# Kernel tuning notes

Measured on AMD Instinct MI355X. Metric: run time of the kernel, lower is better.

The kernel has to match this reference:

```python
import jax, jax.numpy as jnp
import numpy as np

B, S, H, D = 4, 2048, 12, 64
WINDOW = 128          # local_attention window => (w//2, w//2) sliding window
BASE = 16000.0        # rope theta (ProkBert default)
NEG = -1e9


def rotate_half(x):
    x1, x2 = jnp.split(x, 2, axis=-1)
    return jnp.concatenate([-x2, x1], axis=-1)


def setup_inputs() -> dict:
    key = jax.random.key(0)
    k1, = jax.random.split(key, 1)
    qkv = jax.random.normal(k1, (B, S, 3, H, D), dtype=jnp.float32)
    pos = jnp.arange(S)
    inv_freq = 1.0 / (BASE ** (jnp.arange(0, D, 2).astype(jnp.float32) / D))
    freqs = pos[:, None].astype(jnp.float32) * inv_freq[None, :]   # (S, D/2)
    emb = jnp.concatenate([freqs, freqs], axis=-1)                  # (S, D)
    cos = jnp.cos(emb)
    sin = jnp.sin(emb)
    dist = jnp.abs(pos[:, None] - pos[None, :])
    mask = jnp.where(dist <= WINDOW // 2, 0.0, NEG).astype(jnp.float32)[None, None]  # (1,1,S,S)
    return {"qkv": qkv, "cos": cos, "sin": sin, "mask": mask}


def reference(qkv, cos, sin, mask):
    # qkv: (B, S, 3, H, D) -> q/k/v: (B, H, S, D)
    q = jnp.swapaxes(qkv[:, :, 0], 1, 2)
    k = jnp.swapaxes(qkv[:, :, 1], 1, 2)
    v = jnp.swapaxes(qkv[:, :, 2], 1, 2)
    cos_b = cos[None, None]   # (1,1,S,D)
    sin_b = sin[None, None]
    q = q * cos_b + rotate_half(q) * sin_b
    k = k * cos_b + rotate_half(k) * sin_b
    scale = D ** -0.5
    scores = jnp.einsum('bhqd,bhkd->bhqk', q, k) * scale + mask
    w = jax.nn.softmax(scores.astype(jnp.float32), axis=-1).astype(q.dtype)
    out = jnp.einsum('bhqk,bhkd->bhqd', w, v)
    out = jnp.swapaxes(out, 1, 2).reshape(B, S, H * D)  # (B, S, dim)
    return out
```

## Files before the change

kernel.cpp:

```cpp
#include <hip/hip_runtime.h>
#include <hip/hip_bf16.h>
#include <cstdint>


typedef short bf16x8 __attribute__((ext_vector_type(8)));
typedef float f32x4  __attribute__((ext_vector_type(4)));
typedef uint32_t u32x4 __attribute__((ext_vector_type(4)));

#define SLEN   2048
#define NHEAD  12
#define NBATCH 4
#define HD     64
#define WHALF  64
#define QT     64
#define KROWS  192
#define NKC    9
#define VST    68
#define VROWS  96
#define QSCALE 0.18033688011112042f


__device__ __forceinline__ uint32_t cvt_pk(float lo, float hi) {
    uint32_t r;
    asm("v_cvt_pk_bf16_f32 %0, %1, %2" : "=v"(r) : "v"(lo), "v"(hi));
    return r;
}

__global__ __launch_bounds__(256, 3) void prokbert_attn(
        const float* __restrict__ qkv, const float* __restrict__ cosT,
        const float* __restrict__ sinT, float* __restrict__ out)
{
    __shared__ __align__(16) short    sK[KROWS * 64];
    __shared__ __align__(16) uint32_t sV[VROWS * VST];

    const int tid = threadIdx.x;

    const int bid = blockIdx.x;
    const int gid = (bid & 7) * 192 + (bid >> 3);
    const int qt = gid & 31;
    const int hh = gid >> 5;
    const int h = hh % NHEAD, b = hh / NHEAD;

    const int q0 = qt * QT;
    const int kstart = q0 - WHALF;

    const int wv = tid >> 6;
    const int lane = tid & 63;
    const int r = lane & 15, g = lane >> 4;
    const int rx = r & 7;
    const int qrow = q0 + wv * 16 + r;

    f32x4 va[3][2], vb[3][2];
    #pragma unroll
    for (int it = 0; it < 3; ++it) {
        const int j = tid + it * 256;
        const int kp = j >> 3, dd = (j & 7) * 8;
        const int s0 = kstart + 2 * kp, s1 = s0 + 1;
        const f32x4 z = {0.f, 0.f, 0.f, 0.f};
        if ((unsigned)s0 < SLEN) {
            const f32x4* g0 = (const f32x4*)(qkv +
                (((size_t)(b * SLEN + s0) * 3 + 2) * NHEAD + h) * HD + dd);
            va[it][0] = g0[0]; va[it][1] = g0[1];
        } else { va[it][0] = z; va[it][1] = z; }
        if ((unsigned)s1 < SLEN) {
            const f32x4* g1 = (const f32x4*)(qkv +
                (((size_t)(b * SLEN + s1) * 3 + 2) * NHEAD + h) * HD + dd);
            vb[it][0] = g1[0]; vb[it][1] = g1[1];
        } else { vb[it][0] = z; vb[it][1] = z; }
    }

    const int rrb = tid >> 2, c4 = tid & 3, d0 = c4 * 8;

#define LOADK(IT, S) \
    f32x4 xl0##S, xl1##S, xh0##S, xh1##S, cc0##S, cc1##S, ss0##S, ss1##S; \
    { \
        const int s = kstart + rrb + (IT) * 64; \
        if ((unsigned)s < SLEN) { \
            const size_t kbase = (((size_t)(b * SLEN + s) * 3 + 1) * NHEAD + h) * HD; \
            const f32x4* gxl = (const f32x4*)(qkv + kbase + d0); \
            const f32x4* gxh = (const f32x4*)(qkv + kbase + d0 + 32); \
            const f32x4* gc  = (const f32x4*)(cosT + s * HD + d0); \
            const f32x4* gs  = (const f32x4*)(sinT + s * HD + d0); \
            xl0##S = gxl[0]; xl1##S = gxl[1]; \
            xh0##S = gxh[0]; xh1##S = gxh[1]; \
            cc0##S = gc[0];  cc1##S = gc[1]; \
            ss0##S = gs[0];  ss1##S = gs[1]; \
        } else { \
            const f32x4 z = {0.f, 0.f, 0.f, 0.f}; \
            xl0##S = z; xl1##S = z; xh0##S = z; xh1##S = z; \
            cc0##S = z; cc1##S = z; ss0##S = z; ss1##S = z; \
        } \
    }

#define CONVSTOREK(IT, S) \
    { \
        const int rr = rrb + (IT) * 64; \
        u32x4 klo, khi; \
         \
        klo[0] = cvt_pk(xl0##S[0] * cc0##S[0] - xh0##S[0] * ss0##S[0], \
                        xl0##S[1] * cc0##S[1] - xh0##S[1] * ss0##S[1]); \
        klo[1] = cvt_pk(xl0##S[2] * cc0##S[2] - xh0##S[2] * ss0##S[2], \
                        xl0##S[3] * cc0##S[3] - xh0##S[3] * ss0##S[3]); \
        klo[2] = cvt_pk(xl1##S[0] * cc1##S[0] - xh1##S[0] * ss1##S[0], \
                        xl1##S[1] * cc1##S[1] - xh1##S[1] * ss1##S[1]); \
        klo[3] = cvt_pk(xl1##S[2] * cc1##S[2] - xh1##S[2] * ss1##S[2], \
                        xl1##S[3] * cc1##S[3] - xh1##S[3] * ss1##S[3]); \
        khi[0] = cvt_pk(xh0##S[0] * cc0##S[0] + xl0##S[0] * ss0##S[0], \
                        xh0##S[1] * cc0##S[1] + xl0##S[1] * ss0##S[1]); \
        khi[1] = cvt_pk(xh0##S[2] * cc0##S[2] + xl0##S[2] * ss0##S[2], \
                        xh0##S[3] * cc0##S[3] + xl0##S[3] * ss0##S[3]); \
        khi[2] = cvt_pk(xh1##S[0] * cc1##S[0] + xl1##S[0] * ss1##S[0], \
                        xh1##S[1] * cc1##S[1] + xl1##S[1] * ss1##S[1]); \
        khi[3] = cvt_pk(xh1##S[2] * cc1##S[2] + xl1##S[2] * ss1##S[2], \
                        xh1##S[3] * cc1##S[3] + xl1##S[3] * ss1##S[3]); \
        const int sw = rr & 7; \
        *(u32x4*)&sK[rr * 64 + ((c4 ^ sw) << 3)]       = klo; \
        *(u32x4*)&sK[rr * 64 + (((c4 + 4) ^ sw) << 3)] = khi; \
    }

    {
        LOADK(0, a)
        LOADK(1, bb)
        CONVSTOREK(0, a)
        LOADK(2, cc)
        CONVSTOREK(1, bb)
        CONVSTOREK(2, cc)
    }
#undef LOADK
#undef CONVSTOREK

    bf16x8 qf0, qf1;
    {
        const size_t qb = (((size_t)(b * SLEN + qrow) * 3 + 0) * NHEAD + h) * HD;
        const f32x4* ga  = (const f32x4*)(qkv + qb + g * 8);
        const f32x4* gb  = (const f32x4*)(qkv + qb + 32 + g * 8);
        const f32x4* gc0 = (const f32x4*)(cosT + (size_t)qrow * HD + g * 8);
        const f32x4* gs0 = (const f32x4*)(sinT + (size_t)qrow * HD + g * 8);
        f32x4 qa0 = ga[0], qa1 = ga[1], qb0 = gb[0], qb1 = gb[1];
        f32x4 qc0 = gc0[0], qc1 = gc0[1], qs0 = gs0[0], qs1 = gs0[1];
        u32x4 w0, w1;
        w0[0] = cvt_pk((qa0[0] * qc0[0] - qb0[0] * qs0[0]) * QSCALE,
                       (qa0[1] * qc0[1] - qb0[1] * qs0[1]) * QSCALE);
        w0[1] = cvt_pk((qa0[2] * qc0[2] - qb0[2] * qs0[2]) * QSCALE,
                       (qa0[3] * qc0[3] - qb0[3] * qs0[3]) * QSCALE);
        w0[2] = cvt_pk((qa1[0] * qc1[0] - qb1[0] * qs1[0]) * QSCALE,
                       (qa1[1] * qc1[1] - qb1[1] * qs1[1]) * QSCALE);
        w0[3] = cvt_pk((qa1[2] * qc1[2] - qb1[2] * qs1[2]) * QSCALE,
                       (qa1[3] * qc1[3] - qb1[3] * qs1[3]) * QSCALE);
        w1[0] = cvt_pk((qb0[0] * qc0[0] + qa0[0] * qs0[0]) * QSCALE,
                       (qb0[1] * qc0[1] + qa0[1] * qs0[1]) * QSCALE);
        w1[1] = cvt_pk((qb0[2] * qc0[2] + qa0[2] * qs0[2]) * QSCALE,
                       (qb0[3] * qc0[3] + qa0[3] * qs0[3]) * QSCALE);
        w1[2] = cvt_pk((qb1[0] * qc1[0] + qa1[0] * qs1[0]) * QSCALE,
                       (qb1[1] * qc1[1] + qa1[1] * qs1[1]) * QSCALE);
        w1[3] = cvt_pk((qb1[2] * qc1[2] + qa1[2] * qs1[2]) * QSCALE,
                       (qb1[3] * qc1[3] + qa1[3] * qs1[3]) * QSCALE);
        qf0 = __builtin_bit_cast(bf16x8, w0);
        qf1 = __builtin_bit_cast(bf16x8, w1);
    }

    #pragma unroll
    for (int it = 0; it < 3; ++it) {
        const int j = tid + it * 256;
        const int kp = j >> 3, dd = (j & 7) * 8;
        u32x4 w0, w1;
        w0[0] = cvt_pk(va[it][0][0], vb[it][0][0]);
        w0[1] = cvt_pk(va[it][0][1], vb[it][0][1]);
        w0[2] = cvt_pk(va[it][0][2], vb[it][0][2]);
        w0[3] = cvt_pk(va[it][0][3], vb[it][0][3]);
        w1[0] = cvt_pk(va[it][1][0], vb[it][1][0]);
        w1[1] = cvt_pk(va[it][1][1], vb[it][1][1]);
        w1[2] = cvt_pk(va[it][1][2], vb[it][1][2]);
        w1[3] = cvt_pk(va[it][1][3], vb[it][1][3]);
        *(u32x4*)&sV[kp * VST + dd]     = w0;
        *(u32x4*)&sV[kp * VST + dd + 4] = w1;
    }

    __syncthreads();

    u32x4 paw[5];
    float sum = 0.f;
    const int tg = 4 * g;
    #pragma unroll
    for (int kc = 0; kc < NKC; ++kc) {
        const int row = wv * 16 + kc * 16 + r;
        const bf16x8 ka0 = *(const bf16x8*)&sK[row * 64 + ((g ^ rx) << 3)];
        const bf16x8 ka1 = *(const bf16x8*)&sK[row * 64 + (((g + 4) ^ rx) << 3)];
        f32x4 c = {0.f, 0.f, 0.f, 0.f};
        c = __builtin_amdgcn_mfma_f32_16x16x32_bf16(ka0, qf0, c, 0, 0, 0);
        c = __builtin_amdgcn_mfma_f32_16x16x32_bf16(ka1, qf1, c, 0, 0, 0);
        f32x4 e;
        #pragma unroll
        for (int i = 0; i < 4; ++i) {
            float ev = exp2f(c[i]);
            if (kc == 0) ev = (tg + i >= r) ? ev : 0.f;
            if (kc == 8) ev = (tg + i <= r) ? ev : 0.f;
            e[i] = ev;
            sum += ev;
        }
        const uint32_t wlo = cvt_pk(e[0], e[1]);
        const uint32_t whi = cvt_pk(e[2], e[3]);
        if ((kc & 1) == 0) { paw[kc >> 1][0] = wlo; paw[kc >> 1][1] = whi; }
        else               { paw[kc >> 1][2] = wlo; paw[kc >> 1][3] = whi; }
    }
    paw[4][2] = 0; paw[4][3] = 0;

    sum += __shfl_xor(sum, 16);
    sum += __shfl_xor(sum, 32);
    const int oob = max(0, WHALF - qrow) + max(0, qrow - (SLEN - 1 - WHALF));
    const float inv = 1.f / (sum - (float)oob);

    const uint32_t* vptr = &sV[(wv * 8 + 2 * g) * VST + r];
    f32x4 oacc[4] = {{0,0,0,0},{0,0,0,0},{0,0,0,0},{0,0,0,0}};
    #pragma unroll
    for (int kb = 0; kb < 5; ++kb) {
        const bf16x8 pa = __builtin_bit_cast(bf16x8, paw[kb]);
        #pragma unroll
        for (int dc = 0; dc < 4; ++dc) {
            const int base = kb * 16 * VST + dc * 16;
            u32x4 w;
            w[0] = vptr[base];
            w[1] = vptr[base + VST];
            if (kb < 4) {
                w[2] = vptr[base + 8 * VST];
                w[3] = vptr[base + 9 * VST];
            } else {
                w[2] = 0; w[3] = 0;
            }
            const bf16x8 vbf = __builtin_bit_cast(bf16x8, w);
            oacc[dc] = __builtin_amdgcn_mfma_f32_16x16x32_bf16(pa, vbf, oacc[dc], 0, 0, 0);
        }
    }

    #pragma unroll
    for (int i = 0; i < 4; ++i) {
        const float iq = __shfl(inv, g * 4 + i);
        const int qg = q0 + wv * 16 + g * 4 + i;
        float* orow = out + (((size_t)(b * SLEN + qg)) * NHEAD + h) * HD + r;
        orow[0]  = oacc[0][i] * iq;
        orow[16] = oacc[1][i] * iq;
        orow[32] = oacc[2][i] * iq;
        orow[48] = oacc[3][i] * iq;
    }
}

extern "C" void kernel_launch(void* const* d_in, const int* in_sizes, int n_in,
                              void* d_out, int out_size, void* d_ws, size_t ws_size,
                              hipStream_t stream) {
    const float* qkv  = (const float*)d_in[0];
    const float* cosT = (const float*)d_in[1];
    const float* sinT = (const float*)d_in[2];
    float* out = (float*)d_out;
    dim3 grid(32 * NHEAD * NBATCH);
    dim3 block(256);
    hipLaunchKernelGGL(prokbert_attn, grid, block, 0, stream, qkv, cosT, sinT, out);
}
```

Baseline: 27.95 us.

## Split K-rope and V-pack into prep kernel, attention loads pre-swizzled bf16 tiles

Adds a prep kernel that applies RoPE to K and converts K and V to swizzled bf16 layouts in workspace once. The attention kernel then copies these tiles straight into shared memory instead of recomputing rope and conversion for each overlapping 192-row window. This removes the roughly 3x redundant fp32 K/V reads and conversions across neighbouring query tiles. The cost is an extra kernel launch and a workspace write plus read round trip. The old single-kernel path is kept as a fallback when the workspace is too small.

```diff
diff --git a/kernel.cpp b/kernel.cpp
--- a/kernel.cpp
+++ b/kernel.cpp
@@ -15,10 +15,7 @@
 #define QT     64
 #define KROWS  192
 #define NKC    9
-#define VST    68
-#define VROWS  96
 #define QSCALE 0.18033688011112042f
-
 
 __device__ __forceinline__ uint32_t cvt_pk(float lo, float hi) {
     uint32_t r;
@@ -26,12 +23,64 @@
     return r;
 }
 
-__global__ __launch_bounds__(256, 3) void prokbert_attn(
+__global__ __launch_bounds__(256) void prokbert_prep(
         const float* __restrict__ qkv, const float* __restrict__ cosT,
-        const float* __restrict__ sinT, float* __restrict__ out)
+        const float* __restrict__ sinT, short* __restrict__ khat,
+        uint32_t* __restrict__ vhat)
 {
-    __shared__ __align__(16) short    sK[KROWS * 64];
-    __shared__ __align__(16) uint32_t sV[VROWS * VST];
+    const int job = blockIdx.x * 256 + threadIdx.x;
+    if (job < 48 * 2048 * 4) {
+        const int row = job >> 2, c4 = job & 3, d0 = c4 * 8;
+        const int s = row & 2047, hh = row >> 11;
+        const int b = hh / NHEAD, h = hh % NHEAD;
+        const size_t kbase = (((size_t)(b * SLEN + s) * 3 + 1) * NHEAD + h) * HD;
+        const f32x4* gxl = (const f32x4*)(qkv + kbase + d0);
+        const f32x4* gxh = (const f32x4*)(qkv + kbase + d0 + 32);
+        const f32x4* gc  = (const f32x4*)(cosT + s * HD + d0);
+        const f32x4* gs  = (const f32x4*)(sinT + s * HD + d0);
+        const f32x4 xl0 = gxl[0], xl1 = gxl[1], xh0 = gxh[0], xh1 = gxh[1];
+        const f32x4 c0 = gc[0], c1 = gc[1], s0v = gs[0], s1v = gs[1];
+        u32x4 klo, khi;
+        klo[0] = cvt_pk(xl0[0]*c0[0]-xh0[0]*s0v[0], xl0[1]*c0[1]-xh0[1]*s0v[1]);
+        klo[1] = cvt_pk(xl0[2]*c0[2]-xh0[2]*s0v[2], xl0[3]*c0[3]-xh0[3]*s0v[3]);
+        klo[2] = cvt_pk(xl1[0]*c1[0]-xh1[0]*s1v[0], xl1[1]*c1[1]-xh1[1]*s1v[1]);
+        klo[3] = cvt_pk(xl1[2]*c1[2]-xh1[2]*s1v[2], xl1[3]*c1[3]-xh1[3]*s1v[3]);
+        khi[0] = cvt_pk(xh0[0]*c0[0]+xl0[0]*s0v[0], xh0[1]*c0[1]+xl0[1]*s0v[1]);
+        khi[1] = cvt_pk(xh0[2]*c0[2]+xl0[2]*s0v[2], xh0[3]*c0[3]+xl0[3]*s0v[3]);
+        khi[2] = cvt_pk(xh1[0]*c1[0]+xl1[0]*s1v[0], xh1[1]*c1[1]+xl1[1]*s1v[1]);
+        khi[3] = cvt_pk(xh1[2]*c1[2]+xl1[2]*s1v[2], xh1[3]*c1[3]+xl1[3]*s1v[3]);
+        const int sw = s & 7;
+        *(u32x4*)&khat[(size_t)row * 64 + ((c4 ^ sw) << 3)]       = klo;
+        *(u32x4*)&khat[(size_t)row * 64 + (((c4 + 4) ^ sw) << 3)] = khi;
+    } else {
+        const int j2 = job - 48 * 2048 * 4;
+        const int kpg = j2 >> 3, c8 = j2 & 7, d0 = c8 * 8;
+        const int kp = kpg & 1023, hh = kpg >> 10;
+        const int b = hh / NHEAD, h = hh % NHEAD;
+        const int s0 = 2 * kp, s1 = s0 + 1;
+        const f32x4* g0 = (const f32x4*)(qkv +
+            (((size_t)(b * SLEN + s0) * 3 + 2) * NHEAD + h) * HD + d0);
+        const f32x4* g1 = (const f32x4*)(qkv +
+            (((size_t)(b * SLEN + s1) * 3 + 2) * NHEAD + h) * HD + d0);
+        const f32x4 va0 = g0[0], va1 = g0[1], vb0 = g1[0], vb1 = g1[1];
+        u32x4 w0, w1;
+        w0[0] = cvt_pk(va0[0], vb0[0]); w0[1] = cvt_pk(va0[1], vb0[1]);
+        w0[2] = cvt_pk(va0[2], vb0[2]); w0[3] = cvt_pk(va0[3], vb0[3]);
+        w1[0] = cvt_pk(va1[0], vb1[0]); w1[1] = cvt_pk(va1[1], vb1[1]);
+        w1[2] = cvt_pk(va1[2], vb1[2]); w1[3] = cvt_pk(va1[3], vb1[3]);
+        const int col0 = (d0 + 8 * ((kp >> 1) & 3)) & 63;
+        *(u32x4*)&vhat[(size_t)kpg * 64 + col0]     = w0;
+        *(u32x4*)&vhat[(size_t)kpg * 64 + col0 + 4] = w1;
+    }
+}
+
+__global__ __launch_bounds__(256, 3) void prokbert_attn2(
+        const float* __restrict__ qkv, const float* __restrict__ cosT,
+        const float* __restrict__ sinT, const short* __restrict__ khat,
+        const uint32_t* __restrict__ vhat, float* __restrict__ out)
+{
+    __shared__ __align__(16) short    sK2[KROWS * 64];
+    __shared__ __align__(16) uint32_t sV2[96 * 64];
 
     const int tid = threadIdx.x;
 
@@ -43,7 +92,143 @@
 
     const int q0 = qt * QT;
     const int kstart = q0 - WHALF;
-
+    const int kps = kstart / 2;
+
+    const int wv = tid >> 6;
+    const int lane = tid & 63;
+    const int r = lane & 15, g = lane >> 4;
+    const int rx = r & 7;
+    const int qrow = q0 + wv * 16 + r;
+
+    u32x4 kreg[6], vreg[6];
+    #pragma unroll
+    for (int it = 0; it < 6; ++it) {
+        const int ch = wv * 6 + it;
+        const int r0 = kstart + ch * 8;
+        const int kp0 = kps + ch * 4;
+        const u32x4 z = {0, 0, 0, 0};
+        kreg[it] = ((unsigned)r0 <= 2040u)
+            ? *(const u32x4*)&khat[((size_t)hh * SLEN + r0) * 64 + lane * 8]
+            : z;
+        vreg[it] = ((unsigned)kp0 <= 1020u)
+            ? *(const u32x4*)&vhat[((size_t)hh * 1024 + kp0) * 64 + lane * 4]
+            : z;
+    }
+
+    bf16x8 qf0, qf1;
+    {
+        const size_t qb = (((size_t)(b * SLEN + qrow) * 3 + 0) * NHEAD + h) * HD;
+        const f32x4* ga  = (const f32x4*)(qkv + qb + g * 8);
+        const f32x4* gb  = (const f32x4*)(qkv + qb + 32 + g * 8);
+        const f32x4* gc0 = (const f32x4*)(cosT + (size_t)qrow * HD + g * 8);
+        const f32x4* gs0 = (const f32x4*)(sinT + (size_t)qrow * HD + g * 8);
+        const f32x4 qa0 = ga[0], qa1 = ga[1], qb0 = gb[0], qb1 = gb[1];
+        const f32x4 qc0 = gc0[0], qc1 = gc0[1], qs0 = gs0[0], qs1 = gs0[1];
+        u32x4 w0, w1;
+        w0[0] = cvt_pk((qa0[0]*qc0[0]-qb0[0]*qs0[0])*QSCALE, (qa0[1]*qc0[1]-qb0[1]*qs0[1])*QSCALE);
+        w0[1] = cvt_pk((qa0[2]*qc0[2]-qb0[2]*qs0[2])*QSCALE, (qa0[3]*qc0[3]-qb0[3]*qs0[3])*QSCALE);
+        w0[2] = cvt_pk((qa1[0]*qc1[0]-qb1[0]*qs1[0])*QSCALE, (qa1[1]*qc1[1]-qb1[1]*qs1[1])*QSCALE);
+        w0[3] = cvt_pk((qa1[2]*qc1[2]-qb1[2]*qs1[2])*QSCALE, (qa1[3]*qc1[3]-qb1[3]*qs1[3])*QSCALE);
+        w1[0] = cvt_pk((qb0[0]*qc0[0]+qa0[0]*qs0[0])*QSCALE, (qb0[1]*qc0[1]+qa0[1]*qs0[1])*QSCALE);
+        w1[1] = cvt_pk((qb0[2]*qc0[2]+qa0[2]*qs0[2])*QSCALE, (qb0[3]*qc0[3]+qa0[3]*qs0[3])*QSCALE);
+        w1[2] = cvt_pk((qb1[0]*qc1[0]+qa1[0]*qs1[0])*QSCALE, (qb1[1]*qc1[1]+qa1[1]*qs1[1])*QSCALE);
+        w1[3] = cvt_pk((qb1[2]*qc1[2]+qa1[2]*qs1[2])*QSCALE, (qb1[3]*qc1[3]+qa1[3]*qs1[3])*QSCALE);
+        qf0 = __builtin_bit_cast(bf16x8, w0);
+        qf1 = __builtin_bit_cast(bf16x8, w1);
+    }
+
+    #pragma unroll
+    for (int it = 0; it < 6; ++it) {
+        const int ch = wv * 6 + it;
+        *(u32x4*)&sK2[ch * 512 + lane * 8] = kreg[it];
+        *(u32x4*)&sV2[ch * 256 + lane * 4] = vreg[it];
+    }
+    __syncthreads();
+
+    u32x4 paw[5];
+    float sum = 0.f;
+    const int tg = 4 * g;
+    #pragma unroll
+    for (int kc = 0; kc < NKC; ++kc) {
+        const int row = wv * 16 + kc * 16 + r;
+        const bf16x8 ka0 = *(const bf16x8*)&sK2[row * 64 + ((g ^ rx) << 3)];
+        const bf16x8 ka1 = *(const bf16x8*)&sK2[row * 64 + (((g + 4) ^ rx) << 3)];
+        f32x4 c = {0.f, 0.f, 0.f, 0.f};
+        c = __builtin_amdgcn_mfma_f32_16x16x32_bf16(ka0, qf0, c, 0, 0, 0);
+        c = __builtin_amdgcn_mfma_f32_16x16x32_bf16(ka1, qf1, c, 0, 0, 0);
+        f32x4 e;
+        #pragma unroll
+        for (int i = 0; i < 4; ++i) {
+            float ev = exp2f(c[i]);
+            if (kc == 0) ev = (tg + i >= r) ? ev : 0.f;
+            if (kc == 8) ev = (tg + i <= r) ? ev : 0.f;
+            e[i] = ev;
+            sum += ev;
+        }
+        const uint32_t wlo = cvt_pk(e[0], e[1]);
+        const uint32_t whi = cvt_pk(e[2], e[3]);
+        if ((kc & 1) == 0) { paw[kc >> 1][0] = wlo; paw[kc >> 1][1] = whi; }
+        else               { paw[kc >> 1][2] = wlo; paw[kc >> 1][3] = whi; }
+    }
+    paw[4][2] = 0; paw[4][3] = 0;
+
+    sum += __shfl_xor(sum, 16);
+    sum += __shfl_xor(sum, 32);
+    const int oob = max(0, WHALF - qrow) + max(0, qrow - (SLEN - 1 - WHALF));
+    const float inv = 1.f / (sum - (float)oob);
+
+    f32x4 oacc[4] = {{0,0,0,0},{0,0,0,0},{0,0,0,0},{0,0,0,0}};
+    #pragma unroll
+    for (int kb = 0; kb < 5; ++kb) {
+        const bf16x8 pa = __builtin_bit_cast(bf16x8, paw[kb]);
+        const int W = wv * 8 + kb * 16 + 2 * g;
+        #pragma unroll
+        for (int dc = 0; dc < 4; ++dc) {
+            const int col = (dc * 16 + r + 8 * g) & 63;
+            u32x4 w;
+            w[0] = sV2[(W + 0) * 64 + col];
+            w[1] = sV2[(W + 1) * 64 + col];
+            if (kb < 4) {
+                w[2] = sV2[(W + 8) * 64 + col];
+                w[3] = sV2[(W + 9) * 64 + col];
+            } else {
+                w[2] = 0; w[3] = 0;
+            }
+            const bf16x8 vbf = __builtin_bit_cast(bf16x8, w);
+            oacc[dc] = __builtin_amdgcn_mfma_f32_16x16x32_bf16(pa, vbf, oacc[dc], 0, 0, 0);
+        }
+    }
+
+    #pragma unroll
+    for (int i = 0; i < 4; ++i) {
+        const float iq = __shfl(inv, g * 4 + i);
+        const int qg = q0 + wv * 16 + g * 4 + i;
+        float* orow = out + (((size_t)(b * SLEN + qg)) * NHEAD + h) * HD + r;
+        orow[0]  = oacc[0][i] * iq;
+        orow[16] = oacc[1][i] * iq;
+        orow[32] = oacc[2][i] * iq;
+        orow[48] = oacc[3][i] * iq;
+    }
+}
+
+#define VSTM   68
+#define VROWSM 96
+
+__global__ __launch_bounds__(256, 3) void prokbert_attn_mono(
+        const float* __restrict__ qkv, const float* __restrict__ cosT,
+        const float* __restrict__ sinT, float* __restrict__ out)
+{
+    __shared__ __align__(16) short    sK[KROWS * 64];
+    __shared__ __align__(16) uint32_t sV[VROWSM * VSTM];
+
+    const int tid = threadIdx.x;
+    const int bid = blockIdx.x;
+    const int gid = (bid & 7) * 192 + (bid >> 3);
+    const int qt = gid & 31;
+    const int hh = gid >> 5;
+    const int h = hh % NHEAD, b = hh / NHEAD;
+    const int q0 = qt * QT;
+    const int kstart = q0 - WHALF;
     const int wv = tid >> 6;
     const int lane = tid & 63;
     const int r = lane & 15, g = lane >> 4;
@@ -70,7 +255,6 @@
     }
 
     const int rrb = tid >> 2, c4 = tid & 3, d0 = c4 * 8;
-
 #define LOADK(IT, S) \
     f32x4 xl0##S, xl1##S, xh0##S, xh1##S, cc0##S, cc1##S, ss0##S, ss1##S; \
     { \
@@ -91,33 +275,22 @@
             cc0##S = z; cc1##S = z; ss0##S = z; ss1##S = z; \
         } \
     }
-
 #define CONVSTOREK(IT, S) \
     { \
         const int rr = rrb + (IT) * 64; \
         u32x4 klo, khi; \
-         \
-        klo[0] = cvt_pk(xl0##S[0] * cc0##S[0] - xh0##S[0] * ss0##S[0], \
-                        xl0##S[1] * cc0##S[1] - xh0##S[1] * ss0##S[1]); \
-        klo[1] = cvt_pk(xl0##S[2] * cc0##S[2] - xh0##S[2] * ss0##S[2], \
-                        xl0##S[3] * cc0##S[3] - xh0##S[3] * ss0##S[3]); \
-        klo[2] = cvt_pk(xl1##S[0] * cc1##S[0] - xh1##S[0] * ss1##S[0], \
-                        xl1##S[1] * cc1##S[1] - xh1##S[1] * ss1##S[1]); \
-        klo[3] = cvt_pk(xl1##S[2] * cc1##S[2] - xh1##S[2] * ss1##S[2], \
-                        xl1##S[3] * cc1##S[3] - xh1##S[3] * ss1##S[3]); \
-        khi[0] = cvt_pk(xh0##S[0] * cc0##S[0] + xl0##S[0] * ss0##S[0], \
-                        xh0##S[1] * cc0##S[1] + xl0##S[1] * ss0##S[1]); \
-        khi[1] = cvt_pk(xh0##S[2] * cc0##S[2] + xl0##S[2] * ss0##S[2], \
-                        xh0##S[3] * cc0##S[3] + xl0##S[3] * ss0##S[3]); \
-        khi[2] = cvt_pk(xh1##S[0] * cc1##S[0] + xl1##S[0] * ss1##S[0], \
-                        xh1##S[1] * cc1##S[1] + xl1##S[1] * ss1##S[1]); \
-        khi[3] = cvt_pk(xh1##S[2] * cc1##S[2] + xl1##S[2] * ss1##S[2], \
-                        xh1##S[3] * cc1##S[3] + xl1##S[3] * ss1##S[3]); \
+        klo[0] = cvt_pk(xl0##S[0]*cc0##S[0]-xh0##S[0]*ss0##S[0], xl0##S[1]*cc0##S[1]-xh0##S[1]*ss0##S[1]); \
+        klo[1] = cvt_pk(xl0##S[2]*cc0##S[2]-xh0##S[2]*ss0##S[2], xl0##S[3]*cc0##S[3]-xh0##S[3]*ss0##S[3]); \
+        klo[2] = cvt_pk(xl1##S[0]*cc1##S[0]-xh1##S[0]*ss1##S[0], xl1##S[1]*cc1##S[1]-xh1##S[1]*ss1##S[1]); \
+        klo[3] = cvt_pk(xl1##S[2]*cc1##S[2]-xh1##S[2]*ss1##S[2], xl1##S[3]*cc1##S[3]-xh1##S[3]*ss1##S[3]); \
+        khi[0] = cvt_pk(xh0##S[0]*cc0##S[0]+xl0##S[0]*ss0##S[0], xh0##S[1]*cc0##S[1]+xl0##S[1]*ss0##S[1]); \
+        khi[1] = cvt_pk(xh0##S[2]*cc0##S[2]+xl0##S[2]*ss0##S[2], xh0##S[3]*cc0##S[3]+xl0##S[3]*ss0##S[3]); \
+        khi[2] = cvt_pk(xh1##S[0]*cc1##S[0]+xl1##S[0]*ss1##S[0], xh1##S[1]*cc1##S[1]+xl1##S[1]*ss1##S[1]); \
+        khi[3] = cvt_pk(xh1##S[2]*cc1##S[2]+xl1##S[2]*ss1##S[2], xh1##S[3]*cc1##S[3]+xl1##S[3]*ss1##S[3]); \
         const int sw = rr & 7; \
         *(u32x4*)&sK[rr * 64 + ((c4 ^ sw) << 3)]       = klo; \
         *(u32x4*)&sK[rr * 64 + (((c4 + 4) ^ sw) << 3)] = khi; \
     }
-
     {
         LOADK(0, a)
         LOADK(1, bb)
@@ -139,22 +312,14 @@
         f32x4 qa0 = ga[0], qa1 = ga[1], qb0 = gb[0], qb1 = gb[1];
         f32x4 qc0 = gc0[0], qc1 = gc0[1], qs0 = gs0[0], qs1 = gs0[1];
         u32x4 w0, w1;
-        w0[0] = cvt_pk((qa0[0] * qc0[0] - qb0[0] * qs0[0]) * QSCALE,
-                       (qa0[1] * qc0[1] - qb0[1] * qs0[1]) * QSCALE);
-        w0[1] = cvt_pk((qa0[2] * qc0[2] - qb0[2] * qs0[2]) * QSCALE,
-                       (qa0[3] * qc0[3] - qb0[3] * qs0[3]) * QSCALE);
-        w0[2] = cvt_pk((qa1[0] * qc1[0] - qb1[0] * qs1[0]) * QSCALE,
-                       (qa1[1] * qc1[1] - qb1[1] * qs1[1]) * QSCALE);
-        w0[3] = cvt_pk((qa1[2] * qc1[2] - qb1[2] * qs1[2]) * QSCALE,
-                       (qa1[3] * qc1[3] - qb1[3] * qs1[3]) * QSCALE);
-        w1[0] = cvt_pk((qb0[0] * qc0[0] + qa0[0] * qs0[0]) * QSCALE,
-                       (qb0[1] * qc0[1] + qa0[1] * qs0[1]) * QSCALE);
-        w1[1] = cvt_pk((qb0[2] * qc0[2] + qa0[2] * qs0[2]) * QSCALE,
-                       (qb0[3] * qc0[3] + qa0[3] * qs0[3]) * QSCALE);
-        w1[2] = cvt_pk((qb1[0] * qc1[0] + qa1[0] * qs1[0]) * QSCALE,
-                       (qb1[1] * qc1[1] + qa1[1] * qs1[1]) * QSCALE);
-        w1[3] = cvt_pk((qb1[2] * qc1[2] + qa1[2] * qs1[2]) * QSCALE,
-                       (qb1[3] * qc1[3] + qa1[3] * qs1[3]) * QSCALE);
+        w0[0] = cvt_pk((qa0[0]*qc0[0]-qb0[0]*qs0[0])*QSCALE, (qa0[1]*qc0[1]-qb0[1]*qs0[1])*QSCALE);
+        w0[1] = cvt_pk((qa0[2]*qc0[2]-qb0[2]*qs0[2])*QSCALE, (qa0[3]*qc0[3]-qb0[3]*qs0[3])*QSCALE);
+        w0[2] = cvt_pk((qa1[0]*qc1[0]-qb1[0]*qs1[0])*QSCALE, (qa1[1]*qc1[1]-qb1[1]*qs1[1])*QSCALE);
+        w0[3] = cvt_pk((qa1[2]*qc1[2]-qb1[2]*qs1[2])*QSCALE, (qa1[3]*qc1[3]-qb1[3]*qs1[3])*QSCALE);
+        w1[0] = cvt_pk((qb0[0]*qc0[0]+qa0[0]*qs0[0])*QSCALE, (qb0[1]*qc0[1]+qa0[1]*qs0[1])*QSCALE);
+        w1[1] = cvt_pk((qb0[2]*qc0[2]+qa0[2]*qs0[2])*QSCALE, (qb0[3]*qc0[3]+qa0[3]*qs0[3])*QSCALE);
+        w1[2] = cvt_pk((qb1[0]*qc1[0]+qa1[0]*qs1[0])*QSCALE, (qb1[1]*qc1[1]+qa1[1]*qs1[1])*QSCALE);
+        w1[3] = cvt_pk((qb1[2]*qc1[2]+qa1[2]*qs1[2])*QSCALE, (qb1[3]*qc1[3]+qa1[3]*qs1[3])*QSCALE);
         qf0 = __builtin_bit_cast(bf16x8, w0);
         qf1 = __builtin_bit_cast(bf16x8, w1);
     }
@@ -172,10 +337,9 @@
         w1[1] = cvt_pk(va[it][1][1], vb[it][1][1]);
         w1[2] = cvt_pk(va[it][1][2], vb[it][1][2]);
         w1[3] = cvt_pk(va[it][1][3], vb[it][1][3]);
-        *(u32x4*)&sV[kp * VST + dd]     = w0;
-        *(u32x4*)&sV[kp * VST + dd + 4] = w1;
-    }
-
+        *(u32x4*)&sV[kp * VSTM + dd]     = w0;
+        *(u32x4*)&sV[kp * VSTM + dd + 4] = w1;
+    }
     __syncthreads();
 
     u32x4 paw[5];
@@ -210,20 +374,20 @@
     const int oob = max(0, WHALF - qrow) + max(0, qrow - (SLEN - 1 - WHALF));
     const float inv = 1.f / (sum - (float)oob);
 
-    const uint32_t* vptr = &sV[(wv * 8 + 2 * g) * VST + r];
+    const uint32_t* vptr = &sV[(wv * 8 + 2 * g) * VSTM + r];
     f32x4 oacc[4] = {{0,0,0,0},{0,0,0,0},{0,0,0,0},{0,0,0,0}};
     #pragma unroll
     for (int kb = 0; kb < 5; ++kb) {
         const bf16x8 pa = __builtin_bit_cast(bf16x8, paw[kb]);
         #pragma unroll
         for (int dc = 0; dc < 4; ++dc) {
-            const int base = kb * 16 * VST + dc * 16;
+            const int base = kb * 16 * VSTM + dc * 16;
             u32x4 w;
             w[0] = vptr[base];
-            w[1] = vptr[base + VST];
+            w[1] = vptr[base + VSTM];
             if (kb < 4) {
-                w[2] = vptr[base + 8 * VST];
-                w[3] = vptr[base + 9 * VST];
+                w[2] = vptr[base + 8 * VSTM];
+                w[3] = vptr[base + 9 * VSTM];
             } else {
                 w[2] = 0; w[3] = 0;
             }
@@ -251,7 +415,17 @@
     const float* cosT = (const float*)d_in[1];
     const float* sinT = (const float*)d_in[2];
     float* out = (float*)d_out;
-    dim3 grid(32 * NHEAD * NBATCH);
-    dim3 block(256);
-    hipLaunchKernelGGL(prokbert_attn, grid, block, 0, stream, qkv, cosT, sinT, out);
+    const size_t KHAT_BYTES = (size_t)48 * 2048 * 64 * 2;
+    const size_t VHAT_BYTES = (size_t)48 * 1024 * 64 * 4;
+    if (ws_size >= KHAT_BYTES + VHAT_BYTES) {
+        short*    khat = (short*)d_ws;
+        uint32_t* vhat = (uint32_t*)((char*)d_ws + KHAT_BYTES);
+        hipLaunchKernelGGL(prokbert_prep, dim3(3072), dim3(256), 0, stream,
+                           qkv, cosT, sinT, khat, vhat);
+        hipLaunchKernelGGL(prokbert_attn2, dim3(1536), dim3(256), 0, stream,
+                           qkv, cosT, sinT, khat, vhat, out);
+    } else {
+        hipLaunchKernelGGL(prokbert_attn_mono, dim3(1536), dim3(256), 0, stream,
+                           qkv, cosT, sinT, out);
+    }
 }
```

Measured after the change: 35.26 us. 26.1% more time.
